# Kernel optimization log

Hardware: AMD Instinct MI355X
Metric: run time of the kernel (lower is better)

Reference implementation:

```python
import jax, jax.numpy as jnp
import numpy as np

N = 4096

def _backsub(rel_bounds):
    # rel_bounds: list; first entry is ((n,1),(n,1)) input bounds, rest are
    # (out, in+1) relative-bound matrices. Returns exact abs bounds (n,1).
    cur_lb, cur_ub = rel_bounds[-1]
    for prev_lb, prev_ub in reversed(rel_bounds[:-1]):
        bias_row = jnp.zeros((1, prev_lb.shape[-1]), prev_lb.dtype).at[0, -1].set(1.0)
        plb = jnp.concatenate([prev_lb, bias_row], axis=0)
        pub = jnp.concatenate([prev_ub, bias_row], axis=0)
        wp, wn = jax.nn.relu(cur_lb), jax.nn.relu(-cur_lb)
        new_lb = wp @ plb - wn @ pub
        wp, wn = jax.nn.relu(cur_ub), jax.nn.relu(-cur_ub)
        new_ub = wp @ pub - wn @ plb
        cur_lb, cur_ub = new_lb, new_ub
    return cur_lb, cur_ub


def setup_inputs() -> dict:
    key = jax.random.key(0)
    k = jax.random.split(key, 7)
    base = jax.random.normal(k[0], (N, 1), jnp.float32)
    eps = 0.1
    lb0 = base - eps
    ub0 = base + eps
    scale = 0.02  # keep bound magnitudes realistic through the matmul chain
    W1_lb = jax.random.normal(k[1], (N, N + 1), jnp.float32) * scale
    W1_ub = W1_lb + jnp.abs(jax.random.normal(k[2], (N, N + 1), jnp.float32)) * 0.001
    W2_lb = jax.random.normal(k[3], (N, N + 1), jnp.float32) * scale
    W2_ub = W2_lb + jnp.abs(jax.random.normal(k[4], (N, N + 1), jnp.float32)) * 0.001
    alphas = jax.random.uniform(k[5], (N,), jnp.float32)
    return {"lb0": lb0, "ub0": ub0, "W1_lb": W1_lb, "W1_ub": W1_ub,
            "W2_lb": W2_lb, "W2_ub": W2_ub, "alphas": alphas}


def reference(lb0, ub0, W1_lb, W1_ub, W2_lb, W2_ub, alphas):
    prev_lb, prev_ub = _backsub([(lb0, ub0), (W1_lb, W1_ub), (W2_lb, W2_ub)])  # (N,1)
    lb_s = prev_lb[:, 0]
    ub_s = prev_ub[:, 0]
    n = lb_s.shape[0]
    dt = prev_lb.dtype

    alpha = jnp.clip(alphas, 0.0, 1.0)
    alpha = jnp.where(lb_s > 0.0, jnp.ones((), dt), alpha)
    alpha = jnp.where(ub_s <= 0.0, jnp.zeros((), dt), alpha)
    current_lb = jnp.concatenate([jnp.diag(alpha), jnp.zeros((n, 1), dt)], axis=1)

    feps = jnp.finfo(dt).eps
    slope_ub = prev_ub / (prev_ub - prev_lb + feps)          # (N,1)
    slope_ub = jnp.where(prev_lb > 0.0, jnp.ones((), dt), slope_ub)
    slope_ub = jnp.where(prev_ub < 0.0, jnp.zeros((), dt), slope_ub)
    bias_ub = -prev_lb * slope_ub
    bias_ub = jnp.where((prev_lb > 0.0) | (prev_ub < 0.0), jnp.zeros((), dt), bias_ub)
    current_ub = jnp.concatenate([jnp.diag(slope_ub[:, 0]), bias_ub], axis=1)

    # stacked rel_bound appended by the layer: [0]=lower, [1]=upper, each (N, N+1)
    return jnp.stack([current_lb, current_ub])
```

## Files before the change

### kernel.cpp

```cpp
#include <hip/hip_runtime.h>
#include <float.h>

#define N4K 4096
#define NP1 4097

typedef __attribute__((ext_vector_type(4))) float f32x4;
typedef __attribute__((ext_vector_type(8))) short bf16x8;

__device__ __forceinline__ unsigned short f2bf(float x) {
    union { float f; unsigned int u; } v; v.f = x;
    unsigned int r = v.u + 0x7FFFu + ((v.u >> 16) & 1u);
    return (unsigned short)(r >> 16);
}

__device__ __forceinline__ void gload_lds16(const void* g, void* l) {
    __builtin_amdgcn_global_load_lds(
        (const __attribute__((address_space(1))) unsigned int*)g,
        (__attribute__((address_space(3))) unsigned int*)l,
        16, 0, 0);
}

__device__ __forceinline__ void bar() {
    asm volatile("" ::: "memory");
    __builtin_amdgcn_s_barrier();
    asm volatile("" ::: "memory");
}

__global__ __launch_bounds__(256) void prep_A2(const float* __restrict__ W2lb,
                                               const float* __restrict__ W2ub,
                                               const float* __restrict__ mb,
                                               const float* __restrict__ db,
                                               unsigned short* __restrict__ Abf,
                                               float* __restrict__ bias_part) {
    int b = blockIdx.x;
    int chain = b >> 12, i = b & 4095;
    const float* row = (chain ? W2ub : W2lb) + (long long)i * NP1;
    unsigned short* abf_row = Abf + ((long long)chain << 24) + (long long)i * N4K;
    float s = chain ? 1.f : -1.f;
    float part = 0.f;
#pragma unroll 4
    for (int p = 0; p < 16; ++p) {
        int k = threadIdx.x + p * 256;
        float wv = row[k];
        abf_row[k] = f2bf(wv);
        part += wv * mb[k] + s * db[k] * fabsf(wv);
    }
    __shared__ float red[4];
#pragma unroll
    for (int off = 32; off; off >>= 1) part += __shfl_down(part, off);
    if ((threadIdx.x & 63) == 0) red[threadIdx.x >> 6] = part;
    __syncthreads();
    if (threadIdx.x == 0)
        bias_part[b] = red[0] + red[1] + red[2] + red[3] + row[4096];
}

__global__ __launch_bounds__(256) void prep_B(const float* __restrict__ W1lb,
                                              const float* __restrict__ W1ub,
                                              unsigned short* __restrict__ Bmt,
                                              unsigned short* __restrict__ Bdt) {
    __shared__ unsigned short Lm[64 * 65];
    __shared__ unsigned short Ld[64 * 65];
    int j0 = blockIdx.x * 64, k0 = blockIdx.y * 64;
    int t = threadIdx.x;
    int jj = t & 63, kkb = t >> 6;
#pragma unroll 4
    for (int p = 0; p < 16; ++p) {
        int kk = kkb + p * 4;
        long long off = (long long)(k0 + kk) * NP1 + j0 + jj;
        float l = W1lb[off], u = W1ub[off];
        Lm[kk * 65 + jj] = f2bf(0.5f * (l + u));
        Ld[kk * 65 + jj] = f2bf(0.5f * (u - l));
    }
    __syncthreads();
#pragma unroll
    for (int p = 0; p < 2; ++p) {
        int jl = p * 32 + (t >> 3);
        int kl = (t & 7) * 8;
        bf16x8 vm, vd;
#pragma unroll
        for (int i = 0; i < 8; ++i) {
            vm[i] = (short)Lm[(kl + i) * 65 + jl];
            vd[i] = (short)Ld[(kl + i) * 65 + jl];
        }
        *(bf16x8*)&Bmt[(long long)(j0 + jl) * N4K + k0 + kl] = vm;
        *(bf16x8*)&Bdt[(long long)(j0 + jl) * N4K + k0 + kl] = vd;
    }
}

__global__ __launch_bounds__(256) void prep_mbdb(const float* __restrict__ W1lb,
                                                 const float* __restrict__ W1ub,
                                                 float* __restrict__ mb,
                                                 float* __restrict__ db) {
    int k = blockIdx.x * 256 + threadIdx.x;
    if (k < N4K) {
        float l = W1lb[(long long)k * NP1 + 4096];
        float u = W1ub[(long long)k * NP1 + 4096];
        mb[k] = 0.5f * (l + u);
        db[k] = 0.5f * (u - l);
    }
}

__global__ __launch_bounds__(512) void gemm_fused(const unsigned short* __restrict__ Abf,
                                                  const unsigned short* __restrict__ Bmt,
                                                  const unsigned short* __restrict__ Bdt,
                                                  const float* __restrict__ lb0,
                                                  const float* __restrict__ ub0,
                                                  float* __restrict__ pp) {
    __shared__ unsigned short As[3][8192];
    __shared__ unsigned short Bms[3][4096];
    __shared__ unsigned short Bds[3][4096];

    int wg = blockIdx.x;
    int swz = (wg & 7) * 128 + (wg >> 3);
    int rt = swz & 31;
    int ct = swz >> 5;

    int chain = rt >> 4;
    const unsigned short* Aptr = Abf + ((long long)chain << 24) + (long long)(rt & 15) * 256 * N4K;
    const unsigned short* Bmp = Bmt + (long long)ct * 128 * N4K;
    const unsigned short* Bdp = Bdt + (long long)ct * 128 * N4K;

    int tid = threadIdx.x;
    int lane = tid & 63, w = tid >> 6;
    int wr = w >> 1, wc = w & 1;
    int la = lane & 15, kq = lane >> 4;
    int cA = (kq ^ ((la >> 1) & 3)) * 8;

    int sr = tid >> 2;
    int sce = ((tid & 3) ^ ((tid >> 3) & 3)) << 3;
    const unsigned short* aB = Aptr + (long long)sr * N4K + sce;
    const unsigned short* mB = Bmp + (long long)sr * N4K + sce;
    const unsigned short* dB = Bdp + (long long)sr * N4K + sce;
    const long long R128 = 128LL * N4K;
    unsigned w512 = w * 512;

    f32x4 acc[4][4];
#pragma unroll
    for (int m = 0; m < 4; ++m)
#pragma unroll
        for (int n = 0; n < 4; ++n) acc[m][n] = (f32x4){0.f, 0.f, 0.f, 0.f};

#define STAGE(slot, koff)                                              \
    do {                                                               \
        gload_lds16(aB + (koff), &As[slot][w512]);                     \
        gload_lds16(aB + R128 + (koff), &As[slot][4096 + w512]);       \
        gload_lds16(mB + (koff), &Bms[slot][w512]);                    \
        gload_lds16(dB + (koff), &Bds[slot][w512]);                    \
    } while (0)

    STAGE(0, 0);
    STAGE(1, 32);
    asm volatile("s_waitcnt vmcnt(4)" ::: "memory");
    bar();

#define FRAG(arr, s, rb) (*(const bf16x8*)&arr[s][((rb) + la) * 32 + cA])

    int cs = 0, st = 2;
#pragma unroll 1
    for (int t = 0; t < 128; ++t) {
        const bool pf = (t + 2 < 128);
        const long long koff = (long long)(t + 2) * 32;

        bf16x8 a[4], b0[2], b1[2];

#pragma unroll
        for (int m = 0; m < 4; ++m) a[m] = FRAG(As, cs, wr * 64 + m * 16);
#pragma unroll
        for (int n = 0; n < 2; ++n) {
            b0[n] = FRAG(Bms, cs, wc * 64 + n * 16);
            b1[n] = FRAG(Bds, cs, wc * 64 + n * 16);
        }
        if (pf) {
            gload_lds16(aB + koff, &As[st][w512]);
            gload_lds16(aB + R128 + koff, &As[st][4096 + w512]);
        }
        __builtin_amdgcn_s_setprio(1);
#pragma unroll
        for (int m = 0; m < 4; ++m) {
            bf16x8 ax = chain ? (a[m] & (short)0x7FFF) : (a[m] | (short)0x8000);
#pragma unroll
            for (int n = 0; n < 2; ++n) {
                acc[m][n] = __builtin_amdgcn_mfma_f32_16x16x32_bf16(a[m], b0[n], acc[m][n], 0, 0, 0);
                acc[m][n] = __builtin_amdgcn_mfma_f32_16x16x32_bf16(ax, b1[n], acc[m][n], 0, 0, 0);
            }
        }
        __builtin_amdgcn_s_setprio(0);

#pragma unroll
        for (int n = 0; n < 2; ++n) {
            b0[n] = FRAG(Bms, cs, wc * 64 + (n + 2) * 16);
            b1[n] = FRAG(Bds, cs, wc * 64 + (n + 2) * 16);
        }
        if (pf) {
            gload_lds16(mB + koff, &Bms[st][w512]);
            gload_lds16(dB + koff, &Bds[st][w512]);
        }
        __builtin_amdgcn_s_setprio(1);
#pragma unroll
        for (int m = 0; m < 4; ++m) {
            bf16x8 ax = chain ? (a[m] & (short)0x7FFF) : (a[m] | (short)0x8000);
#pragma unroll
            for (int n = 0; n < 2; ++n) {
                acc[m][n + 2] = __builtin_amdgcn_mfma_f32_16x16x32_bf16(a[m], b0[n], acc[m][n + 2], 0, 0, 0);
                acc[m][n + 2] = __builtin_amdgcn_mfma_f32_16x16x32_bf16(ax, b1[n], acc[m][n + 2], 0, 0, 0);
            }
        }
        __builtin_amdgcn_s_setprio(0);

        if (pf) asm volatile("s_waitcnt vmcnt(4)" ::: "memory");
        else    asm volatile("s_waitcnt vmcnt(0)" ::: "memory");
        bar();

        cs = (cs == 2) ? 0 : cs + 1;
        st = (st == 2) ? 0 : st + 1;
    }
#undef FRAG
#undef STAGE

    float s = chain ? 1.f : -1.f;
    float rowpart[4][4];
#pragma unroll
    for (int m = 0; m < 4; ++m)
#pragma unroll
        for (int r = 0; r < 4; ++r) rowpart[m][r] = 0.f;

    int jbase = ct * 128 + wc * 64;
#pragma unroll
    for (int n = 0; n < 4; ++n) {
        int j = jbase + n * 16 + la;
        float l0 = lb0[j], u0 = ub0[j];
        float mj = 0.5f * (l0 + u0);
        float sdj = s * 0.5f * (u0 - l0);
#pragma unroll
        for (int m = 0; m < 4; ++m)
#pragma unroll
            for (int r = 0; r < 4; ++r) {
                float v = acc[m][n][r];
                rowpart[m][r] += v * mj + sdj * fabsf(v);
            }
    }
    long long rowg = (long long)chain * N4K + (rt & 15) * 256 + wr * 64 + kq * 4;
    long long slice = (long long)(ct * 2 + wc) * 8192;
#pragma unroll
    for (int m = 0; m < 4; ++m)
#pragma unroll
        for (int r = 0; r < 4; ++r) {
            float v = rowpart[m][r];
            v += __shfl_xor(v, 1);
            v += __shfl_xor(v, 2);
            v += __shfl_xor(v, 4);
            v += __shfl_xor(v, 8);
            if (la == 0) pp[slice + rowg + m * 16 + r] = v;
        }
}

__global__ __launch_bounds__(256) void reduce_pp(const float* __restrict__ pp,
                                                 const float* __restrict__ bias_part,
                                                 float* __restrict__ prev) {
    int j = blockIdx.x * 256 + threadIdx.x;
    float s = bias_part[j];
#pragma unroll 8
    for (int c = 0; c < 64; ++c) s += pp[(long long)c * 8192 + j];
    prev[j] = s;
}

__global__ __launch_bounds__(256) void epilogue(const float* __restrict__ prev,
                                                const float* __restrict__ alphas,
                                                float* __restrict__ out) {
    int i = blockIdx.x * 256 + threadIdx.x;
    if (i >= N4K) return;
    float lb = prev[i], ub = prev[N4K + i];
    float a = fminf(fmaxf(alphas[i], 0.f), 1.f);
    if (lb > 0.f) a = 1.f;
    if (ub <= 0.f) a = 0.f;
    float slope = ub / (ub - lb + FLT_EPSILON);
    if (lb > 0.f) slope = 1.f;
    if (ub < 0.f) slope = 0.f;
    float bias = -lb * slope;
    if (lb > 0.f || ub < 0.f) bias = 0.f;
    long long P = NP1, half = (long long)N4K * NP1;
    out[(long long)i * P + i] = a;
    out[half + (long long)i * P + i] = slope;
    out[half + (long long)i * P + 4096] = bias;
}

extern "C" void kernel_launch(void* const* d_in, const int* in_sizes, int n_in,
                              void* d_out, int out_size, void* d_ws, size_t ws_size,
                              hipStream_t stream) {
    const float* lb0    = (const float*)d_in[0];
    const float* ub0    = (const float*)d_in[1];
    const float* W1lb   = (const float*)d_in[2];
    const float* W1ub   = (const float*)d_in[3];
    const float* W2lb   = (const float*)d_in[4];
    const float* W2ub   = (const float*)d_in[5];
    const float* alphas = (const float*)d_in[6];

    char* ws = (char*)d_ws;
    float* bias_part = (float*)ws;
    float* mb   = (float*)(ws + 32768);
    float* db   = (float*)(ws + 49152);
    float* prev = (float*)(ws + 32768);
    unsigned short* Abf = (unsigned short*)(ws + 65536);
    unsigned short* Bmt = (unsigned short*)(ws + 65536 + 67108864);
    unsigned short* Bdt = (unsigned short*)(ws + 65536 + 100663296);
    size_t need = 65536ULL + 67108864ULL + 2ULL * 33554432ULL;
    if (ws_size < need) return;

    float* pp = (float*)d_out;

    (void)hipMemsetAsync(d_out, 0, (size_t)out_size * 4, stream);

    prep_mbdb<<<16, 256, 0, stream>>>(W1lb, W1ub, mb, db);
    prep_A2<<<8192, 256, 0, stream>>>(W2lb, W2ub, mb, db, Abf, bias_part);
    prep_B<<<dim3(64, 64), 256, 0, stream>>>(W1lb, W1ub, Bmt, Bdt);
    gemm_fused<<<1024, 512, 0, stream>>>(Abf, Bmt, Bdt, lb0, ub0, pp);
    reduce_pp<<<32, 256, 0, stream>>>(pp, bias_part, prev);
    (void)hipMemsetAsync(d_out, 0, 64 * 8192 * 4, stream);
    epilogue<<<16, 256, 0, stream>>>(prev, alphas, (float*)d_out);
}
```

Baseline: 717.0 us.

## Deepen LDS prefetch to four stages and split MFMA phases by operand

Grows the shared-memory ring from three to four k-slices so three tiles are in flight, and adjusts the vmcnt waits to match. The inner loop is reorganised into two phases: first all mean-B MFMAs against the A fragments, then all delta-B MFMAs with the sign-masked A. Extra workgroup barriers are placed around each phase to interleave global-to-LDS prefetch with compute. The aim is to hide more global-load latency, at the cost of more LDS (now 128KB per block) and extra barrier synchronisation each iteration.

```diff
diff --git a/kernel.cpp b/kernel.cpp
--- a/kernel.cpp
+++ b/kernel.cpp
@@ -106,9 +106,9 @@
                                                   const float* __restrict__ lb0,
                                                   const float* __restrict__ ub0,
                                                   float* __restrict__ pp) {
-    __shared__ unsigned short As[3][8192];
-    __shared__ unsigned short Bms[3][4096];
-    __shared__ unsigned short Bds[3][4096];
+    __shared__ unsigned short As[4][8192];
+    __shared__ unsigned short Bms[4][4096];
+    __shared__ unsigned short Bds[4][4096];
 
     int wg = blockIdx.x;
     int swz = (wg & 7) * 128 + (wg >> 3);
@@ -140,82 +140,70 @@
 #pragma unroll
         for (int n = 0; n < 4; ++n) acc[m][n] = (f32x4){0.f, 0.f, 0.f, 0.f};
 
-#define STAGE(slot, koff)                                              \
-    do {                                                               \
-        gload_lds16(aB + (koff), &As[slot][w512]);                     \
-        gload_lds16(aB + R128 + (koff), &As[slot][4096 + w512]);       \
-        gload_lds16(mB + (koff), &Bms[slot][w512]);                    \
-        gload_lds16(dB + (koff), &Bds[slot][w512]);                    \
-    } while (0)
-
-    STAGE(0, 0);
-    STAGE(1, 32);
-    asm volatile("s_waitcnt vmcnt(4)" ::: "memory");
+#pragma unroll
+    for (int q = 0; q < 3; ++q) {
+        long long koff = (long long)q * 32;
+        gload_lds16(aB + koff, &As[q][w512]);
+        gload_lds16(aB + R128 + koff, &As[q][4096 + w512]);
+        gload_lds16(mB + koff, &Bms[q][w512]);
+        gload_lds16(dB + koff, &Bds[q][w512]);
+    }
+    asm volatile("s_waitcnt vmcnt(8)" ::: "memory");
     bar();
 
 #define FRAG(arr, s, rb) (*(const bf16x8*)&arr[s][((rb) + la) * 32 + cA])
 
-    int cs = 0, st = 2;
 #pragma unroll 1
     for (int t = 0; t < 128; ++t) {
-        const bool pf = (t + 2 < 128);
-        const long long koff = (long long)(t + 2) * 32;
-
-        bf16x8 a[4], b0[2], b1[2];
-
-#pragma unroll
-        for (int m = 0; m < 4; ++m) a[m] = FRAG(As, cs, wr * 64 + m * 16);
-#pragma unroll
-        for (int n = 0; n < 2; ++n) {
-            b0[n] = FRAG(Bms, cs, wc * 64 + n * 16);
-            b1[n] = FRAG(Bds, cs, wc * 64 + n * 16);
-        }
+        const int s = t & 3, ss = (t + 3) & 3;
+        const bool pf = (t + 3 < 128);
+        const long long koff = (long long)(t + 3) * 32;
+
+        bf16x8 a[4], b[4];
+
+#pragma unroll
+        for (int m = 0; m < 4; ++m) a[m] = FRAG(As, s, wr * 64 + m * 16);
+#pragma unroll
+        for (int n = 0; n < 4; ++n) b[n] = FRAG(Bms, s, wc * 64 + n * 16);
         if (pf) {
-            gload_lds16(aB + koff, &As[st][w512]);
-            gload_lds16(aB + R128 + koff, &As[st][4096 + w512]);
-        }
+            gload_lds16(aB + koff, &As[ss][w512]);
+            gload_lds16(aB + R128 + koff, &As[ss][4096 + w512]);
+        }
+        bar();
+        asm volatile("s_waitcnt lgkmcnt(0)" ::: "memory");
+        __builtin_amdgcn_s_setprio(1);
+#pragma unroll
+        for (int m = 0; m < 4; ++m)
+#pragma unroll
+            for (int n = 0; n < 4; ++n)
+                acc[m][n] = __builtin_amdgcn_mfma_f32_16x16x32_bf16(a[m], b[n], acc[m][n], 0, 0, 0);
+        __builtin_amdgcn_s_setprio(0);
+        bar();
+
+#pragma unroll
+        for (int n = 0; n < 4; ++n) b[n] = FRAG(Bds, s, wc * 64 + n * 16);
+        if (pf) {
+            gload_lds16(mB + koff, &Bms[ss][w512]);
+            gload_lds16(dB + koff, &Bds[ss][w512]);
+        }
+        bar();
+        asm volatile("s_waitcnt lgkmcnt(0)" ::: "memory");
         __builtin_amdgcn_s_setprio(1);
 #pragma unroll
         for (int m = 0; m < 4; ++m) {
             bf16x8 ax = chain ? (a[m] & (short)0x7FFF) : (a[m] | (short)0x8000);
 #pragma unroll
-            for (int n = 0; n < 2; ++n) {
-                acc[m][n] = __builtin_amdgcn_mfma_f32_16x16x32_bf16(a[m], b0[n], acc[m][n], 0, 0, 0);
-                acc[m][n] = __builtin_amdgcn_mfma_f32_16x16x32_bf16(ax, b1[n], acc[m][n], 0, 0, 0);
-            }
+            for (int n = 0; n < 4; ++n)
+                acc[m][n] = __builtin_amdgcn_mfma_f32_16x16x32_bf16(ax, b[n], acc[m][n], 0, 0, 0);
         }
         __builtin_amdgcn_s_setprio(0);
 
-#pragma unroll
-        for (int n = 0; n < 2; ++n) {
-            b0[n] = FRAG(Bms, cs, wc * 64 + (n + 2) * 16);
-            b1[n] = FRAG(Bds, cs, wc * 64 + (n + 2) * 16);
-        }
-        if (pf) {
-            gload_lds16(mB + koff, &Bms[st][w512]);
-            gload_lds16(dB + koff, &Bds[st][w512]);
-        }
-        __builtin_amdgcn_s_setprio(1);
-#pragma unroll
-        for (int m = 0; m < 4; ++m) {
-            bf16x8 ax = chain ? (a[m] & (short)0x7FFF) : (a[m] | (short)0x8000);
-#pragma unroll
-            for (int n = 0; n < 2; ++n) {
-                acc[m][n + 2] = __builtin_amdgcn_mfma_f32_16x16x32_bf16(a[m], b0[n], acc[m][n + 2], 0, 0, 0);
-                acc[m][n + 2] = __builtin_amdgcn_mfma_f32_16x16x32_bf16(ax, b1[n], acc[m][n + 2], 0, 0, 0);
-            }
-        }
-        __builtin_amdgcn_s_setprio(0);
-
-        if (pf) asm volatile("s_waitcnt vmcnt(4)" ::: "memory");
-        else    asm volatile("s_waitcnt vmcnt(0)" ::: "memory");
+        if (t < 125)       asm volatile("s_waitcnt vmcnt(8)" ::: "memory");
+        else if (t == 125) asm volatile("s_waitcnt vmcnt(4)" ::: "memory");
+        else               asm volatile("s_waitcnt vmcnt(0)" ::: "memory");
         bar();
-
-        cs = (cs == 2) ? 0 : cs + 1;
-        st = (st == 2) ? 0 : st + 1;
     }
 #undef FRAG
-#undef STAGE
 
     float s = chain ? 1.f : -1.f;
     float rowpart[4][4];
```

New measurement: 735.4 us. 1.03x slower.
